# Kernel optimization log

Measured on AMD Instinct MI355X. Metric: run time of the kernel, lower is better.

The kernel has to match this reference:

```python
import jax, jax.numpy as jnp
import numpy as np

B, T, C = 64, 256, 1024
H, DH = 16, 64           # n_heads, head_dim (C == H*DH)
NP, WS = 16, 2           # n_patches per side, window_size (T == NP*NP)
EPS = 1e-5


def setup_inputs() -> dict:
    key = jax.random.key(0)
    ks = jax.random.split(key, 8)
    s = lambda k, shape, fan: jax.random.normal(k, shape, jnp.float32) * (fan ** -0.5)
    return dict(
        x=jax.random.normal(ks[0], (B, T, C), jnp.float32),
        ln1_g=jnp.ones((C,), jnp.float32), ln1_b=jnp.zeros((C,), jnp.float32),
        Wq=s(ks[1], (H, C, DH), C), Wk=s(ks[2], (H, C, DH), C), Wv=s(ks[3], (H, C, DH), C),
        Wp=s(ks[4], (C, C), C), bp=jnp.zeros((C,), jnp.float32),
        ln2_g=jnp.ones((C,), jnp.float32), ln2_b=jnp.zeros((C,), jnp.float32),
        W1=s(ks[5], (C, C), C), b1=jnp.zeros((C,), jnp.float32),
        W2=s(ks[6], (C, C), C), b2=jnp.zeros((C,), jnp.float32))


def _ln(x, g, b):
    m = x.mean(-1, keepdims=True)
    v = x.var(-1, keepdims=True)
    return (x - m) * jax.lax.rsqrt(v + EPS) * g + b


def reference(x, ln1_g, ln1_b, Wq, Wk, Wv, Wp, bp, ln2_g, ln2_b, W1, b1, W2, b2):
    h = NP // WS                      # windows per side = 8
    nw = h * h                        # 64 windows of WS*WS = 4 tokens
    xn = _ln(x, ln1_g, ln1_b)
    # window partition: [B, T, C] -> [B*nw, WS*WS, C]
    xw = (xn.reshape(B, h, WS, h, WS, C)
            .transpose(0, 1, 3, 2, 4, 5)
            .reshape(B * nw, WS * WS, C))
    # all-heads batched QKV (original loops over heads; math identical since
    # torch.cat of per-head outputs == head-axis stack then reshape)
    q = jnp.einsum('ntc,hcd->nhtd', xw, Wq)
    k = jnp.einsum('ntc,hcd->nhtd', xw, Wk)
    v = jnp.einsum('ntc,hcd->nhtd', xw, Wv)
    # NOTE: scale is C**-0.5 with C = d_model (faithful to source, not head_dim)
    wei = jax.nn.softmax(jnp.einsum('nhqd,nhkd->nhqk', q, k) * (C ** -0.5), axis=-1)
    att = jnp.einsum('nhqk,nhkd->nhqd', wei, v)
    att = att.transpose(0, 2, 1, 3).reshape(B * nw, WS * WS, C)
    att = att @ Wp + bp
    # residual adds the LayerNorm-ed, window-partitioned x (faithful quirk)
    xr = xw + att
    # reverse window partition -> [B, T, C]
    xr = (xr.reshape(B, h, h, WS, WS, C)
            .transpose(0, 1, 3, 2, 4, 5)
            .reshape(B, T, C))
    ff = jax.nn.gelu(_ln(xr, ln2_g, ln2_b) @ W1 + b1, approximate=False) @ W2 + b2
    return xr + ff
```

## Files before the change

### kernel.cpp

```cpp
#include <hip/hip_runtime.h>
#include <math.h>

typedef unsigned short u16;
typedef unsigned int   u32;

using f32x4  = __attribute__((ext_vector_type(4))) float;
using s16x8  = __attribute__((ext_vector_type(8))) short;
using u16x8  = __attribute__((ext_vector_type(8))) unsigned short;

__device__ __forceinline__ u16 f2b(float f) {
    u32 u = __float_as_uint(f);
    u += 0x7FFFu + ((u >> 16) & 1u);
    return (u16)(u >> 16);
}
__device__ __forceinline__ float b2f(u16 u) { return __uint_as_float(((u32)u) << 16); }

__device__ __forceinline__ int natrow(int R) {
    int b = R >> 8, r8 = R & 255, w = r8 >> 2, t = r8 & 3;
    return (b << 8) + ((((w >> 3) << 1) + (t >> 1)) << 4) + ((w & 7) << 1) + (t & 1);
}

__device__ __forceinline__ void gll16(const void* g, void* l) {
    __builtin_amdgcn_global_load_lds(
        (const __attribute__((address_space(1))) void*)g,
        (__attribute__((address_space(3))) void*)l, 16, 0, 0);
}

__device__ __forceinline__ void transpose_body(
    const float* __restrict__ in, u16* __restrict__ out, int R, int C)
{
    __shared__ float tile[32][33];
    const int tx = threadIdx.x, ty = threadIdx.y;
    const int c  = blockIdx.x * 32 + tx;
    const int r0 = blockIdx.y * 32;
#pragma unroll
    for (int i = 0; i < 32; i += 8) tile[ty + i][tx] = in[(size_t)(r0 + ty + i) * C + c];
    __syncthreads();
    const int orow0 = blockIdx.x * 32;
    const int ocol  = r0 + tx;
#pragma unroll
    for (int i = 0; i < 32; i += 8)
        out[(size_t)(orow0 + ty + i) * R + ocol] = f2b(tile[tx][ty + i]);
}

__global__ __launch_bounds__(256) void transpose_qkv(
    const float* __restrict__ Wq, const float* __restrict__ Wk,
    const float* __restrict__ Wv, u16* __restrict__ out)
{
    const int z = blockIdx.z;
    const float* in = (z < 16 ? Wq : z < 32 ? Wk : Wv) + (size_t)(z & 15) * 65536;
    transpose_body(in, out + (size_t)z * 65536, 1024, 64);
}

__global__ __launch_bounds__(256) void transpose_pw(
    const float* __restrict__ Wp, const float* __restrict__ W1,
    const float* __restrict__ W2, u16* __restrict__ out)
{
    const int z = blockIdx.z;
    const float* in = z == 0 ? Wp : z == 1 ? W1 : W2;
    transpose_body(in, out + (size_t)z * 1048576, 1024, 1024);
}

template<int MAP, int BIN>
__global__ __launch_bounds__(256) void ln_kernel(
    const void* __restrict__ X, const float* __restrict__ g, const float* __restrict__ bta,
    u16* __restrict__ outB)
{
    const int R   = blockIdx.x;
    const int src = MAP ? natrow(R) : R;
    float x0, x1, x2, x3;
    if (BIN) {
        const ushort4 r = ((const ushort4*)((const u16*)X + (size_t)src * 1024))[threadIdx.x];
        x0 = b2f(r.x); x1 = b2f(r.y); x2 = b2f(r.z); x3 = b2f(r.w);
    } else {
        const float4 r = ((const float4*)((const float*)X + (size_t)src * 1024))[threadIdx.x];
        x0 = r.x; x1 = r.y; x2 = r.z; x3 = r.w;
    }
    float s  = x0 + x1 + x2 + x3;
    float s2 = x0 * x0 + x1 * x1 + x2 * x2 + x3 * x3;
#pragma unroll
    for (int o = 32; o; o >>= 1) { s += __shfl_xor(s, o); s2 += __shfl_xor(s2, o); }
    __shared__ float red[8];
    const int w = threadIdx.x >> 6, l = threadIdx.x & 63;
    if (l == 0) { red[w] = s; red[w + 4] = s2; }
    __syncthreads();
    s  = red[0] + red[1] + red[2] + red[3];
    s2 = red[4] + red[5] + red[6] + red[7];
    const float mean = s * (1.f / 1024.f);
    const float var  = s2 * (1.f / 1024.f) - mean * mean;
    const float rinv = rsqrtf(var + 1e-5f);
    const float4 gv = ((const float4*)g)[threadIdx.x];
    const float4 bv = ((const float4*)bta)[threadIdx.x];
    ((ushort4*)(outB + (size_t)R * 1024))[threadIdx.x] = make_ushort4(
        f2b((x0 - mean) * rinv * gv.x + bv.x), f2b((x1 - mean) * rinv * gv.y + bv.y),
        f2b((x2 - mean) * rinv * gv.z + bv.z), f2b((x3 - mean) * rinv * gv.w + bv.w));
}

template<int MODE>
__global__ __launch_bounds__(512, 2) void gemm256(
    const u16* __restrict__ A, const u16* __restrict__ Bt,
    const float* __restrict__ bias, const void* __restrict__ resid,
    void* __restrict__ Out, int M, int N, int K, int LDA, int NB)
{
    extern __shared__ char lds[];
    const int NT = K >> 6;
    const int nblk = gridDim.x;
    const int lb = (blockIdx.x & 7) * (nblk >> 3) + (blockIdx.x >> 3);
    const int mb = lb / NB, nb = lb - mb * NB;
    const int row0 = mb * 256, col0 = nb * 256;
    const int tid = threadIdx.x;
    const int w = tid >> 6, l = tid & 63;
    const int wr = w >> 2, wc = w & 3;
    const int lr = l & 15, kg = l >> 4;
    const int xs = (lr & 7) << 4;
    const int koff[2] = { (kg * 16) ^ xs, (64 + kg * 16) ^ xs };
    const int abase_l = wr * 8192 + lr * 128;
    const int bbase_l = wc * 4096 + lr * 128;

    f32x4 acc[2][2][4][2] = {};
    s16x8 a0[4][2], a1[4][2], b[2][2];

    auto stage = [&](int ts, int item) {
        if (ts >= NT) return;
        const int d = ts & 1;
        const int isB = item & 1, h = item >> 1;
        char* lbase = lds + (isB ? 65536 : 0) + d * 32768 + h * 16384;
        const u16* gptr = isB ? Bt : A;
        const int ld = isB ? K : LDA;
        const int blk0 = (isB ? col0 : row0) + h * 128;
#pragma unroll
        for (int j = 0; j < 2; ++j) {
            const int p = j * 512 + tid;
            const int q = p ^ ((p >> 3) & 7);
            const int grow = blk0 + (q >> 3);
            const int gcol = ts * 64 + (q & 7) * 8;
            gll16(gptr + (size_t)grow * ld + gcol, lbase + (j * 8 + w) * 1024);
        }
    };

#define LOAD_A(dst, qm) do { \
    _Pragma("unroll") for (int kk = 0; kk < 2; ++kk) \
    _Pragma("unroll") for (int i = 0; i < 4; ++i) \
        dst[i][kk] = *(const s16x8*)(Ab + (qm) * 16384 + abase_l + i * 2048 + koff[kk]); \
} while (0)
#define LOAD_B(qn) do { \
    _Pragma("unroll") for (int kk = 0; kk < 2; ++kk) \
    _Pragma("unroll") for (int n = 0; n < 2; ++n) \
        b[n][kk] = *(const s16x8*)(Bb + (qn) * 16384 + bbase_l + n * 2048 + koff[kk]); \
} while (0)
#define SYNC_PRE do { \
    __builtin_amdgcn_sched_barrier(0); \
    __builtin_amdgcn_s_barrier(); \
    asm volatile("s_waitcnt lgkmcnt(0)" ::: "memory"); \
    __builtin_amdgcn_sched_barrier(0); \
} while (0)
#define MFMA_Q(qm, qn, aa) do { \
    __builtin_amdgcn_s_setprio(1); \
    _Pragma("unroll") for (int kk = 0; kk < 2; ++kk) \
    _Pragma("unroll") for (int i = 0; i < 4; ++i) \
    _Pragma("unroll") for (int n = 0; n < 2; ++n) \
        acc[qm][qn][i][n] = __builtin_amdgcn_mfma_f32_16x16x32_bf16( \
            aa[i][kk], b[n][kk], acc[qm][qn][i][n], 0, 0, 0); \
    __builtin_amdgcn_s_setprio(0); \
    __builtin_amdgcn_sched_barrier(0); \
} while (0)
#define SYNC_POST(p) do { \
    if ((p) == 0) { \
        if (t == NT - 1) asm volatile("s_waitcnt vmcnt(0)" ::: "memory"); \
        else            asm volatile("s_waitcnt vmcnt(4)" ::: "memory"); \
    } else if ((p) == 3 && t < NT - 1) { \
        asm volatile("s_waitcnt vmcnt(4)" ::: "memory"); \
    } \
    __builtin_amdgcn_s_barrier(); \
    __builtin_amdgcn_sched_barrier(0); \
} while (0)

    stage(0, 0); stage(0, 1); stage(0, 2); stage(0, 3);
    asm volatile("s_waitcnt vmcnt(4)" ::: "memory");
    __builtin_amdgcn_s_barrier();

    for (int t = 0; t < NT; ++t) {
        const char* Ab = lds + (t & 1) * 32768;
        const char* Bb = lds + 65536 + (t & 1) * 32768;
        LOAD_A(a0, 0); LOAD_B(0);
        stage(t + 1, 0); stage(t + 1, 1);
        SYNC_PRE; MFMA_Q(0, 0, a0); SYNC_POST(0);
        LOAD_A(a1, 1);
        stage(t + 1, 2); stage(t + 1, 3);
        SYNC_PRE; MFMA_Q(1, 0, a1); SYNC_POST(1);
        LOAD_B(1);
        SYNC_PRE; MFMA_Q(1, 1, a1); SYNC_POST(2);
        MFMA_Q(0, 1, a0); SYNC_POST(3);
    }
#undef LOAD_A
#undef LOAD_B
#undef SYNC_PRE
#undef MFMA_Q
#undef SYNC_POST

#pragma unroll
    for (int qm = 0; qm < 2; ++qm)
#pragma unroll
    for (int i = 0; i < 4; ++i) {
        const int grb = row0 + qm * 128 + wr * 64 + i * 16 + kg * 4;
#pragma unroll
        for (int qn = 0; qn < 2; ++qn)
#pragma unroll
        for (int n = 0; n < 2; ++n) {
            const int gc = col0 + qn * 128 + wc * 32 + n * 16 + lr;
#pragma unroll
            for (int j = 0; j < 4; ++j) {
                const int gr = grb + j;
                const float v = acc[qm][qn][i][n][j];
                if (MODE == 0) {
                    ((u16*)Out)[(size_t)gr * N + gc] = f2b(v);
                } else if (MODE == 2) {
                    const float tt = v + bias[gc];
                    ((u16*)Out)[(size_t)gr * N + gc] = f2b(0.5f * tt * (1.f + erff(tt * 0.70710678118f)));
                } else if (MODE == 3) {
                    ((float*)Out)[(size_t)natrow(gr) * N + gc] =
                        v + bias[gc] + b2f(((const u16*)resid)[(size_t)gr * N + gc]);
                } else {
                    ((u16*)Out)[(size_t)gr * N + gc] =
                        f2b(v + bias[gc] + b2f(((const u16*)resid)[(size_t)gr * N + gc]));
                }
            }
        }
    }
}

__global__ __launch_bounds__(256) void attn_kernel(u16* __restrict__ QKV)
{
    const int w = threadIdx.x >> 6, l = threadIdx.x & 63;
    const int n = blockIdx.x * 4 + w;
    u16* base = QKV + (size_t)n * 4 * 3072;
    const float scale = 0.03125f;
#pragma unroll
    for (int c = 0; c < 2; ++c) {
        const int col = c * 512 + l * 8;
        u16x8 qr[4], kr[4], vr[4];
#pragma unroll
        for (int t = 0; t < 4; ++t) {
            qr[t] = *(const u16x8*)(base + t * 3072 + col);
            kr[t] = *(const u16x8*)(base + t * 3072 + 1024 + col);
            vr[t] = *(const u16x8*)(base + t * 3072 + 2048 + col);
        }
        float qf[4][8], kf[4][8];
#pragma unroll
        for (int t = 0; t < 4; ++t)
#pragma unroll
            for (int j = 0; j < 8; ++j) { qf[t][j] = b2f(qr[t][j]); kf[t][j] = b2f(kr[t][j]); }
        float s[4][4];
#pragma unroll
        for (int t = 0; t < 4; ++t)
#pragma unroll
            for (int u = 0; u < 4; ++u) {
                float p = qf[t][0] * kf[u][0];
#pragma unroll
                for (int j = 1; j < 8; ++j) p += qf[t][j] * kf[u][j];
                p += __shfl_xor(p, 1); p += __shfl_xor(p, 2); p += __shfl_xor(p, 4);
                s[t][u] = p * scale;
            }
#pragma unroll
        for (int t = 0; t < 4; ++t) {
            const float m = fmaxf(fmaxf(s[t][0], s[t][1]), fmaxf(s[t][2], s[t][3]));
            const float e0 = expf(s[t][0] - m), e1 = expf(s[t][1] - m);
            const float e2 = expf(s[t][2] - m), e3 = expf(s[t][3] - m);
            const float inv = 1.f / (e0 + e1 + e2 + e3);
            u16x8 o;
#pragma unroll
            for (int j = 0; j < 8; ++j)
                o[j] = f2b((e0 * b2f(vr[0][j]) + e1 * b2f(vr[1][j]) +
                            e2 * b2f(vr[2][j]) + e3 * b2f(vr[3][j])) * inv);
            *(u16x8*)(base + t * 3072 + col) = o;
        }
    }
}

extern "C" void kernel_launch(void* const* d_in, const int* in_sizes, int n_in,
                              void* d_out, int out_size, void* d_ws, size_t ws_size,
                              hipStream_t stream)
{
    const float* x    = (const float*)d_in[0];
    const float* ln1g = (const float*)d_in[1];
    const float* ln1b = (const float*)d_in[2];
    const float* Wq   = (const float*)d_in[3];
    const float* Wk   = (const float*)d_in[4];
    const float* Wv   = (const float*)d_in[5];
    const float* Wp   = (const float*)d_in[6];
    const float* bp   = (const float*)d_in[7];
    const float* ln2g = (const float*)d_in[8];
    const float* ln2b = (const float*)d_in[9];
    const float* W1   = (const float*)d_in[10];
    const float* b1   = (const float*)d_in[11];
    const float* W2   = (const float*)d_in[12];
    const float* b2   = (const float*)d_in[13];
    float* out = (float*)d_out;

    char* ws = (char*)d_ws;
    const size_t MB = 1024 * 1024;
    u16* xr_b  = (u16*)ws;
    u16* xw_b  = (u16*)(ws + 32 * MB);
    u16* qkv   = (u16*)(ws + 64 * MB);
    u16* h1b   = (u16*)(ws + 64 * MB);
    u16* ln2bf = (u16*)(ws + 160 * MB);
    u16* WqkvT = (u16*)(ws + 192 * MB);
    u16* WpT   = (u16*)(ws + 198 * MB);
    u16* W1T   = WpT + (1u << 20);
    u16* W2T   = W1T + (1u << 20);

    hipFuncSetAttribute((const void*)gemm256<0>, hipFuncAttributeMaxDynamicSharedMemorySize, 131072);
    hipFuncSetAttribute((const void*)gemm256<2>, hipFuncAttributeMaxDynamicSharedMemorySize, 131072);
    hipFuncSetAttribute((const void*)gemm256<3>, hipFuncAttributeMaxDynamicSharedMemorySize, 131072);
    hipFuncSetAttribute((const void*)gemm256<5>, hipFuncAttributeMaxDynamicSharedMemorySize, 131072);

    const int M = 16384, K = 1024;
    dim3 tpb(32, 8);
    transpose_qkv<<<dim3(2, 32, 48), tpb, 0, stream>>>(Wq, Wk, Wv, WqkvT);
    transpose_pw <<<dim3(32, 32, 3), tpb, 0, stream>>>(Wp, W1, W2, WpT);

    ln_kernel<1, 0><<<16384, 256, 0, stream>>>(x, ln1g, ln1b, xw_b);

    gemm256<0><<<768, 512, 131072, stream>>>(xw_b, WqkvT, nullptr, nullptr, qkv, M, 3072, K, K, 12);

    attn_kernel<<<1024, 256, 0, stream>>>(qkv);

    gemm256<5><<<256, 512, 131072, stream>>>(qkv, WpT, bp, xw_b, xr_b, M, 1024, K, 3072, 4);

    ln_kernel<0, 1><<<16384, 256, 0, stream>>>(xr_b, ln2g, ln2b, ln2bf);

    gemm256<2><<<256, 512, 131072, stream>>>(ln2bf, W1T, b1, nullptr, h1b, M, 1024, K, K, 4);

    gemm256<3><<<256, 512, 131072, stream>>>(h1b, W2T, b2, xr_b, out, M, 1024, K, K, 4);
}
```

Baseline: 322.1 us.

## Restructure GEMM main loop to issue all fragment loads upfront with one barrier

The bf16 GEMM K-loop now reads all A and B fragments from LDS at the start of each iteration into separate register sets (b0/b1). It then issues every global-to-LDS prefetch for the next tile at once and staggers the MFMA quadrants behind progressive lgkmcnt waits. The four barriers per iteration become a single vmcnt(0) plus barrier at the end, which is meant to cut synchronization stalls and let LDS reads overlap with MFMA work. The trade-offs are extra B-fragment registers and a full wait on the next tile's global loads every iteration, with no partial vmcnt overlap.

```diff
diff --git a/kernel.cpp b/kernel.cpp
--- a/kernel.cpp
+++ b/kernel.cpp
@@ -118,7 +118,7 @@
     const int bbase_l = wc * 4096 + lr * 128;
 
     f32x4 acc[2][2][4][2] = {};
-    s16x8 a0[4][2], a1[4][2], b[2][2];
+    s16x8 a0[4][2], a1[4][2], b0[2][2], b1[2][2];
 
     auto stage = [&](int ts, int item) {
         if (ts >= NT) return;
@@ -143,60 +143,58 @@
     _Pragma("unroll") for (int i = 0; i < 4; ++i) \
         dst[i][kk] = *(const s16x8*)(Ab + (qm) * 16384 + abase_l + i * 2048 + koff[kk]); \
 } while (0)
-#define LOAD_B(qn) do { \
+#define LOAD_B(dst, qn) do { \
     _Pragma("unroll") for (int kk = 0; kk < 2; ++kk) \
     _Pragma("unroll") for (int n = 0; n < 2; ++n) \
-        b[n][kk] = *(const s16x8*)(Bb + (qn) * 16384 + bbase_l + n * 2048 + koff[kk]); \
+        dst[n][kk] = *(const s16x8*)(Bb + (qn) * 16384 + bbase_l + n * 2048 + koff[kk]); \
 } while (0)
-#define SYNC_PRE do { \
-    __builtin_amdgcn_sched_barrier(0); \
-    __builtin_amdgcn_s_barrier(); \
-    asm volatile("s_waitcnt lgkmcnt(0)" ::: "memory"); \
-    __builtin_amdgcn_sched_barrier(0); \
-} while (0)
-#define MFMA_Q(qm, qn, aa) do { \
+#define MFMA_Q(qm, qn, aa, bb) do { \
     __builtin_amdgcn_s_setprio(1); \
     _Pragma("unroll") for (int kk = 0; kk < 2; ++kk) \
     _Pragma("unroll") for (int i = 0; i < 4; ++i) \
     _Pragma("unroll") for (int n = 0; n < 2; ++n) \
         acc[qm][qn][i][n] = __builtin_amdgcn_mfma_f32_16x16x32_bf16( \
-            aa[i][kk], b[n][kk], acc[qm][qn][i][n], 0, 0, 0); \
+            aa[i][kk], bb[n][kk], acc[qm][qn][i][n], 0, 0, 0); \
     __builtin_amdgcn_s_setprio(0); \
     __builtin_amdgcn_sched_barrier(0); \
 } while (0)
-#define SYNC_POST(p) do { \
-    if ((p) == 0) { \
-        if (t == NT - 1) asm volatile("s_waitcnt vmcnt(0)" ::: "memory"); \
-        else            asm volatile("s_waitcnt vmcnt(4)" ::: "memory"); \
-    } else if ((p) == 3 && t < NT - 1) { \
-        asm volatile("s_waitcnt vmcnt(4)" ::: "memory"); \
-    } \
-    __builtin_amdgcn_s_barrier(); \
+#define WAIT_LGKM(n) do { \
+    asm volatile("s_waitcnt lgkmcnt(" #n ")" ::: "memory"); \
     __builtin_amdgcn_sched_barrier(0); \
 } while (0)
 
     stage(0, 0); stage(0, 1); stage(0, 2); stage(0, 3);
-    asm volatile("s_waitcnt vmcnt(4)" ::: "memory");
+    asm volatile("s_waitcnt vmcnt(0)" ::: "memory");
     __builtin_amdgcn_s_barrier();
 
     for (int t = 0; t < NT; ++t) {
         const char* Ab = lds + (t & 1) * 32768;
         const char* Bb = lds + 65536 + (t & 1) * 32768;
-        LOAD_A(a0, 0); LOAD_B(0);
-        stage(t + 1, 0); stage(t + 1, 1);
-        SYNC_PRE; MFMA_Q(0, 0, a0); SYNC_POST(0);
+        LOAD_A(a0, 0); LOAD_B(b0, 0);
+        __builtin_amdgcn_sched_barrier(0);
         LOAD_A(a1, 1);
-        stage(t + 1, 2); stage(t + 1, 3);
-        SYNC_PRE; MFMA_Q(1, 0, a1); SYNC_POST(1);
-        LOAD_B(1);
-        SYNC_PRE; MFMA_Q(1, 1, a1); SYNC_POST(2);
-        MFMA_Q(0, 1, a0); SYNC_POST(3);
+        __builtin_amdgcn_sched_barrier(0);
+        LOAD_B(b1, 1);
+        __builtin_amdgcn_sched_barrier(0);
+        stage(t + 1, 0); stage(t + 1, 1); stage(t + 1, 2); stage(t + 1, 3);
+        __builtin_amdgcn_sched_barrier(0);
+        WAIT_LGKM(12);
+        MFMA_Q(0, 0, a0, b0);
+        WAIT_LGKM(4);
+        MFMA_Q(1, 0, a1, b0);
+        WAIT_LGKM(0);
+        MFMA_Q(1, 1, a1, b1);
+        MFMA_Q(0, 1, a0, b1);
+        if (t < NT - 1) {
+            asm volatile("s_waitcnt vmcnt(0)" ::: "memory");
+            __builtin_amdgcn_s_barrier();
+            __builtin_amdgcn_sched_barrier(0);
+        }
     }
 #undef LOAD_A
 #undef LOAD_B
-#undef SYNC_PRE
 #undef MFMA_Q
-#undef SYNC_POST
+#undef WAIT_LGKM
 
 #pragma unroll
     for (int qm = 0; qm < 2; ++qm)
```

New measurement: 312.8 us. -2.9%, faster.
